# Kernel tuning notes

Hardware: AMD Instinct MI355X
Metric: run time of the kernel (lower is better)

## Reference

```python
import jax, jax.numpy as jnp
import numpy as np

EPS = 1e-6
POSE_W, DEPTH_W, POINTS_W, NORMAL_W = 1.0, 1.0, 1.0, 0.1
DEPTH_MIN = 1e-6


def mat_to_quat(M):
    # pytorch3d-style robust rotation-matrix -> quaternion (w,x,y,z)
    m00, m01, m02 = M[..., 0, 0], M[..., 0, 1], M[..., 0, 2]
    m10, m11, m12 = M[..., 1, 0], M[..., 1, 1], M[..., 1, 2]
    m20, m21, m22 = M[..., 2, 0], M[..., 2, 1], M[..., 2, 2]
    q_abs = jnp.sqrt(jnp.maximum(jnp.stack([
        1.0 + m00 + m11 + m22,
        1.0 + m00 - m11 - m22,
        1.0 - m00 + m11 - m22,
        1.0 - m00 - m11 + m22], axis=-1), 0.0))
    cand = jnp.stack([
        jnp.stack([q_abs[..., 0] ** 2, m21 - m12, m02 - m20, m10 - m01], -1),
        jnp.stack([m21 - m12, q_abs[..., 1] ** 2, m10 + m01, m02 + m20], -1),
        jnp.stack([m02 - m20, m10 + m01, q_abs[..., 2] ** 2, m12 + m21], -1),
        jnp.stack([m10 - m01, m20 + m02, m21 + m12, q_abs[..., 3] ** 2], -1),
    ], axis=-2)  # [...,4,4]
    cand = cand / (2.0 * jnp.maximum(q_abs[..., None], 0.1))
    best = jnp.argmax(q_abs, axis=-1)
    quat = jnp.take_along_axis(cand, best[..., None, None], axis=-2)[..., 0, :]
    return jnp.where(quat[..., 0:1] < 0, -quat, quat)


def pose_encoding(extri, intr, H, W):
    # extri [B,S,3,4] -> [B,S,9] = absT(3) + quat(4) + fov_h,fov_w
    T = extri[..., :3, 3]
    quat = mat_to_quat(extri[..., :3, :3])
    fov_h = 2.0 * jnp.arctan((H / 2.0) / intr[..., 1, 1])
    fov_w = 2.0 * jnp.arctan((W / 2.0) / intr[..., 0, 0])
    return jnp.concatenate([T, quat, fov_h[..., None], fov_w[..., None]], axis=-1)


def align_depth_scale(dp, dg, vm):
    # batched masked-median scale; dp detached by caller. Returns (aligned_gt, scales[B,S])
    B, S, H, W = dg.shape
    dpf, dgf = dp.reshape(B, S, H * W), dg.reshape(B, S, H * W)
    m = vm.reshape(B, S, H * W)
    m2 = m & jnp.isfinite(dpf) & (dpf > EPS)
    ratio = dpf / jnp.maximum(dgf, EPS)
    fm = m2 & jnp.isfinite(ratio)
    msum = m2.sum(-1)
    fcnt = fm.sum(-1)
    r = jnp.sort(jnp.where(fm, ratio, jnp.inf), axis=-1)
    idx = jnp.maximum((fcnt - 1) // 2, 0)  # torch lower median
    med = jnp.take_along_axis(r, idx[..., None], axis=-1)[..., 0]
    scale = jnp.clip(med, 1e-3, 1e3)
    scale = jnp.where((msum < 16) | (fcnt == 0), jnp.ones_like(scale), scale)
    return dg * scale[..., None, None], scale


def _cam_grid(depth, intr):
    B, S, H, W = depth.shape
    ys, xs = jnp.meshgrid(jnp.arange(H, dtype=depth.dtype),
                          jnp.arange(W, dtype=depth.dtype), indexing='ij')
    fx = intr[..., 0, 0][..., None, None]
    fy = intr[..., 1, 1][..., None, None]
    cx = intr[..., 0, 2][..., None, None]
    cy = intr[..., 1, 2][..., None, None]
    x = (xs - cx) / jnp.maximum(fx, EPS) * depth
    y = (ys - cy) / jnp.maximum(fy, EPS) * depth
    return jnp.stack([x, y, depth], axis=-1)  # [B,S,H,W,3]


def depth_to_normals(depth, intr):
    pts = _cam_grid(depth, intr)
    fx_diff = pts[..., 1:-1, 2:, :] - pts[..., 1:-1, :-2, :]
    fy_diff = pts[..., 2:, 1:-1, :] - pts[..., :-2, 1:-1, :]
    core = jnp.cross(fy_diff, fx_diff)
    core = core / jnp.maximum(jnp.linalg.norm(core, axis=-1, keepdims=True), EPS)
    return jnp.zeros_like(pts).at[..., 1:-1, 1:-1, :].set(core)


def depth_to_world_points(depth, intr, pose):
    cam_pts = _cam_grid(depth, intr)
    rot = pose[..., :3, :3]
    trans = pose[..., :3, 3]
    return jnp.einsum('bsij,bshwj->bshwi', rot, cam_pts) + trans[..., None, None, :]


def masked_l1(pred, target, mask):
    mask = mask.astype(pred.dtype)
    return ((pred - target) * mask).__abs__().sum() / jnp.maximum(mask.sum(), 1.0)


def masked_cosine_loss(pred, target, mask):
    pred = pred / jnp.maximum(jnp.linalg.norm(pred, axis=-1, keepdims=True), EPS)
    target = target / jnp.maximum(jnp.linalg.norm(target, axis=-1, keepdims=True), EPS)
    cos = jnp.clip((pred * target).sum(-1), -1.0, 1.0)
    m = mask.astype(cos.dtype)
    return ((1.0 - cos) * m).sum() / jnp.maximum(m.sum(), 1.0)


def smooth_l1(pred, target):
    d = jnp.abs(pred - target)
    return jnp.mean(jnp.where(d < 1.0, 0.5 * d * d, d - 0.5))


def supervised_loss(depth_pred, points_pred, pose_pred, depth_gt, intrinsics,
                    pose_matrix_gt, valid_mask):
    B, S, H, W = depth_gt.shape
    vm = valid_mask & jnp.isfinite(depth_gt) & (depth_gt > DEPTH_MIN)
    depth_gt_aligned, scales = align_depth_scale(
        jax.lax.stop_gradient(depth_pred), depth_gt, vm)
    points_gt = depth_to_world_points(depth_gt_aligned, intrinsics, pose_matrix_gt)
    points_mask = jnp.broadcast_to(vm[..., None], points_gt.shape)
    # normal mask: zero-out 1-pixel border
    border = jnp.zeros((H, W), dtype=bool).at[1:-1, 1:-1].set(True)
    normal_mask = vm & border
    pred_normals = depth_to_normals(depth_pred, intrinsics)
    gt_normals = depth_to_normals(depth_gt, intrinsics)
    normal_loss = masked_cosine_loss(pred_normals, gt_normals, normal_mask)
    pose_gt = pose_encoding(pose_matrix_gt[..., :3, :], intrinsics, H, W)
    pose_gt = pose_gt.at[..., :3].multiply(scales[..., None])
    depth_loss = masked_l1(depth_pred, depth_gt_aligned, vm)
    points_loss = masked_l1(points_pred, points_gt, points_mask)
    pose_loss = smooth_l1(pose_pred, pose_gt)
    return (POSE_W * pose_loss + DEPTH_W * depth_loss
            + POINTS_W * points_loss + NORMAL_W * normal_loss)


def setup_inputs() -> dict:
    key = jax.random.key(0)
    ks = jax.random.split(key, 7)
    B, S, H, W = 4, 8, 384, 512
    depth_gt = jax.random.uniform(ks[0], (B, S, H, W), minval=0.5, maxval=10.0)
    depth_pred = depth_gt * jax.random.uniform(ks[1], (B, S, H, W), minval=0.8, maxval=1.2)
    points_pred = jax.random.normal(ks[2], (B, S, H, W, 3))
    pose_pred = 0.1 * jax.random.normal(ks[3], (B, S, 9))
    intr = jnp.broadcast_to(jnp.array([[500.0, 0.0, W / 2.0],
                                       [0.0, 500.0, H / 2.0],
                                       [0.0, 0.0, 1.0]], jnp.float32), (B, S, 3, 3))
    q, _ = jnp.linalg.qr(jax.random.normal(ks[4], (B, S, 3, 3)))
    R = q * jnp.sign(jnp.linalg.det(q))[..., None, None]  # det=+1
    t = jax.random.normal(ks[5], (B, S, 3))
    top = jnp.concatenate([R, t[..., None]], axis=-1)
    bottom = jnp.broadcast_to(jnp.array([0.0, 0.0, 0.0, 1.0], jnp.float32), (B, S, 1, 4))
    pose_matrix_gt = jnp.concatenate([top, bottom], axis=-2)
    valid_mask = jax.random.uniform(ks[6], (B, S, H, W)) > 0.05
    return {"depth_pred": depth_pred, "points_pred": points_pred,
            "pose_pred": pose_pred, "depth_gt": depth_gt,
            "intrinsics": intr, "pose_matrix_gt": pose_matrix_gt,
            "valid_mask": valid_mask}


def reference(depth_pred, points_pred, pose_pred, depth_gt, intrinsics,
              pose_matrix_gt, valid_mask):
    return supervised_loss(depth_pred, points_pred, pose_pred, depth_gt,
                           intrinsics, pose_matrix_gt, valid_mask)
```

## Files before the change

### kernel.cpp

```cpp
#include <hip/hip_runtime.h>
#include <stdint.h>

#define H_ 384
#define W_ 512
#define HW_ (H_ * W_)
#define NIMG 32
#define EPSF 1e-6f
#define HBLK 16
#define HTHR 512
#define PXB (HW_ / HBLK)
#define CITER (PXB / (HTHR * 4))
#define MBLK 96
#define NPARTS (MBLK * NIMG)
#define SENT 0xFFFFFFFFu

#define OFF_MSUM   0
#define OFF_FCNT   32
#define OFF_KREM1  64
#define OFF_PREF1  96
#define OFF_POSE   128
#define OFF_PMF    160
#define OFF_PNC    1184
#define OFF_PART   2208
#define OFF_PHA    11424
#define OFF_PHB    (OFF_PHA + NIMG*HBLK*2048)

__device__ __forceinline__ bool finitef(float x) {
    return ((__float_as_uint(x) >> 23) & 0xFFu) != 0xFFu;
}

__global__ __launch_bounds__(HTHR) void hist0_k(
    const float* __restrict__ dp, const float* __restrict__ dg,
    const uint8_t* __restrict__ vmask, uint32_t* __restrict__ ws)
{
    __shared__ uint32_t lh[2048];
    __shared__ int sm[8], sf[8];
    const int img = blockIdx.y, blk = blockIdx.x, t = threadIdx.x;
    for (int b = t; b < 2048; b += HTHR) lh[b] = 0;
    __syncthreads();

    const size_t base = (size_t)img * HW_;
    const float* dpi = dp + base;
    const float* dgi = dg + base;
    const uint8_t* mi = vmask + base;

    int m2c = 0, fmc = 0;

    for (int c = 0; c < CITER; ++c) {
        const int pix = blk * PXB + c * (HTHR * 4) + t * 4;
        const float4 v_dp = *reinterpret_cast<const float4*>(dpi + pix);
        const float4 v_dg = *reinterpret_cast<const float4*>(dgi + pix);
        const uchar4 v_m  = *reinterpret_cast<const uchar4*>(mi + pix);
        const float dpa[4] = {v_dp.x, v_dp.y, v_dp.z, v_dp.w};
        const float dga[4] = {v_dg.x, v_dg.y, v_dg.z, v_dg.w};
        const uint8_t ma[4] = {v_m.x, v_m.y, v_m.z, v_m.w};
        int bins[4]; bool fms[4];
#pragma unroll
        for (int e = 0; e < 4; ++e) {
            const float dgv = dga[e], dpv = dpa[e];
            const bool vm = ma[e] && finitef(dgv) && (dgv > 1e-6f);
            const bool m2 = vm && finitef(dpv) && (dpv > EPSF);
            const float ratio = dpv / fmaxf(dgv, EPSF);
            const bool fm = m2 && finitef(ratio);
            m2c += (int)m2; fmc += (int)fm;
            const uint32_t key = fm ? __float_as_uint(ratio) : SENT;
            bins[e] = (int)(key >> 21);
            fms[e] = fm;
        }

#pragma unroll
        for (int e = 0; e < 4; ++e) {
            const bool fm = fms[e];
            const int bin = bins[e];
            unsigned long long todo = __ballot(fm);
            while (todo) {
                const int lead = (int)__ffsll(todo) - 1;
                const int lbin = __shfl(bin, lead);
                const unsigned long long same = __ballot(fm && (bin == lbin));
                if ((t & 63) == lead)
                    atomicAdd(&lh[lbin], (uint32_t)__popcll(same));
                todo &= ~same;
            }
        }
    }

    for (int o = 32; o > 0; o >>= 1) { m2c += __shfl_down(m2c, o); fmc += __shfl_down(fmc, o); }
    if ((t & 63) == 0) { sm[t >> 6] = m2c; sf[t >> 6] = fmc; }
    __syncthreads();
    if (t == 0) {
        int M = 0, F = 0;
        for (int w = 0; w < 8; ++w) { M += sm[w]; F += sf[w]; }
        int* pmf = (int*)(ws + OFF_PMF) + (img * HBLK + blk) * 2;
        pmf[0] = M; pmf[1] = F;
    }

    uint32_t* phb = ws + OFF_PHA + (size_t)(img * HBLK + blk) * 2048;
    for (int b = t; b < 2048; b += HTHR) phb[b] = lh[b];
}

__global__ __launch_bounds__(HTHR) void histp1_k(
    const float* __restrict__ dp, const float* __restrict__ dg,
    const uint8_t* __restrict__ vmask, const float* __restrict__ intr,
    uint32_t* __restrict__ ws)
{
    __shared__ uint32_t lh[256];
    __shared__ uint32_t wsum[8];
    __shared__ int s_bin, s_krem, s_msum, s_fcnt;
    __shared__ float sI[4];
    __shared__ float sns[8]; __shared__ int snc[8];
    const int img = blockIdx.y, blk = blockIdx.x, t = threadIdx.x;

    const uint32_t* pin = ws + OFF_PHA + (size_t)img * HBLK * 2048;
    uint32_t local[4];
#pragma unroll
    for (int c = 0; c < 4; ++c) local[c] = 0;
    for (int b = 0; b < HBLK; ++b) {
        const uint32_t* row = pin + b * 2048 + t * 4;
#pragma unroll
        for (int c = 0; c < 4; ++c) local[c] += row[c];
    }
    const uint32_t cs = local[0] + local[1] + local[2] + local[3];

    uint32_t v = cs;
#pragma unroll
    for (int o = 1; o < 64; o <<= 1) {
        const uint32_t u = __shfl_up(v, o);
        if ((t & 63) >= o) v += u;
    }
    if ((t & 63) == 63) wsum[t >> 6] = v;
    if (t == 0) {
        s_bin = 0; s_krem = 0;
        const int* pmf = (const int*)(ws + OFF_PMF) + img * HBLK * 2;
        int M = 0, F = 0;
        for (int b = 0; b < HBLK; ++b) { M += pmf[2 * b]; F += pmf[2 * b + 1]; }
        s_msum = M; s_fcnt = F;
        sI[0] = 1.0f / fmaxf(intr[img * 9 + 0], EPSF);
        sI[1] = 1.0f / fmaxf(intr[img * 9 + 4], EPSF);
        sI[2] = intr[img * 9 + 2];
        sI[3] = intr[img * 9 + 5];
    }
    __syncthreads();
    uint32_t woff = 0;
    for (int w = 0; w < (t >> 6); ++w) woff += wsum[w];
    const uint32_t incl = woff + v;
    const uint32_t excl = incl - cs;

    const uint32_t k = (uint32_t)max((s_fcnt - 1) / 2, 0);
    if (k >= excl && k < incl) {
        uint32_t cum = excl;
#pragma unroll
        for (int c = 0; c < 4; ++c) {
            if (cum + local[c] > k) { s_bin = t * 4 + c; s_krem = (int)(k - cum); break; }
            cum += local[c];
        }
    }
    __syncthreads();
    if (t == 0 && blk == 0) {
        ((int*)(ws + OFF_MSUM))[img] = s_msum;
        ((int*)(ws + OFF_FCNT))[img] = s_fcnt;
        (ws + OFF_PREF1)[img] = (uint32_t)s_bin << 21;
        ((int*)(ws + OFF_KREM1))[img] = s_krem;
    }
    const uint32_t pm = (uint32_t)s_bin;
    const float inv_fx = sI[0], inv_fy = sI[1], cx = sI[2], cy = sI[3];

    if (t < 256) lh[t] = 0;
    __syncthreads();

    const size_t base = (size_t)img * HW_;
    const float* dpi = dp + base;
    const float* dgi = dg + base;
    float nsum = 0.0f; int ncc = 0;

    for (int c = 0; c < CITER; ++c) {
        const int pix = blk * PXB + c * (HTHR * 4) + t * 4;
        const int i = pix >> 9;
        const int j0 = pix & 511;
        const float4 v_dp = *reinterpret_cast<const float4*>(dpi + pix);
        const float4 v_dg = *reinterpret_cast<const float4*>(dgi + pix);
        const uchar4 v_m  = *reinterpret_cast<const uchar4*>(vmask + base + pix);

        const int im = (i > 0) ? i - 1 : 0;
        const int ip = (i < H_ - 1) ? i + 1 : i;
        const int jme = (j0 > 0) ? j0 - 1 : 0;
        const int jpe = (j0 + 4 < W_) ? j0 + 4 : W_ - 1;
        const float4 dpU = *reinterpret_cast<const float4*>(dpi + im * W_ + j0);
        const float4 dpD = *reinterpret_cast<const float4*>(dpi + ip * W_ + j0);
        const float4 dgU = *reinterpret_cast<const float4*>(dgi + im * W_ + j0);
        const float4 dgD = *reinterpret_cast<const float4*>(dgi + ip * W_ + j0);
        const float dpLe = dpi[i * W_ + jme], dpRe = dpi[i * W_ + jpe];
        const float dgLe = dgi[i * W_ + jme], dgRe = dgi[i * W_ + jpe];

        const float dpa[4] = {v_dp.x, v_dp.y, v_dp.z, v_dp.w};
        const float dga[4] = {v_dg.x, v_dg.y, v_dg.z, v_dg.w};
        const float dpUa[4] = {dpU.x, dpU.y, dpU.z, dpU.w};
        const float dpDa[4] = {dpD.x, dpD.y, dpD.z, dpD.w};
        const float dgUa[4] = {dgU.x, dgU.y, dgU.z, dgU.w};
        const float dgDa[4] = {dgD.x, dgD.y, dgD.z, dgD.w};
        const uint8_t ma[4] = {v_m.x, v_m.y, v_m.z, v_m.w};

        const float ay = ((float)i - cy) * inv_fy;
        const bool row_int = (i >= 1) && (i <= H_ - 2);

#pragma unroll
        for (int e = 0; e < 4; ++e) {
            const int j = j0 + e;
            const float dgv = dga[e], dpv = dpa[e];
            const bool vm = ma[e] && finitef(dgv) && (dgv > 1e-6f);
            const bool m2 = vm && finitef(dpv) && (dpv > EPSF);
            const float ratio = dpv / fmaxf(dgv, EPSF);
            const bool fm = m2 && finitef(ratio);
            const uint32_t key = fm ? __float_as_uint(ratio) : SENT;
            if ((key >> 21) == pm)
                atomicAdd(&lh[(key >> 13) & 255u], 1u);

            const bool nm = vm && row_int && (j >= 1) && (j <= W_ - 2);
            const float pdL = (e == 0) ? dpLe : dpa[e - 1];
            const float pdR = (e == 3) ? dpRe : dpa[e + 1];
            const float gdL = (e == 0) ? dgLe : dga[e - 1];
            const float gdR = (e == 3) ? dgRe : dga[e + 1];
            const float pdU = dpUa[e], pdD = dpDa[e];
            const float gdU = dgUa[e], gdD = dgDa[e];
            const float ax = ((float)j - cx) * inv_fx;

            const float dRLp = pdR - pdL, dDUp = pdD - pdU;
            const float Ap = inv_fy * (pdD + pdU);
            const float Bp = inv_fx * (pdR + pdL);
            const float cpx = dRLp * Ap;
            const float cpy = dDUp * Bp;
            const float cpz = -(Ap * Bp + ax * cpx + ay * cpy);
            const float dRLg = gdR - gdL, dDUg = gdD - gdU;
            const float Ag = inv_fy * (gdD + gdU);
            const float Bg = inv_fx * (gdR + gdL);
            const float cgx = dRLg * Ag;
            const float cgy = dDUg * Bg;
            const float cgz = -(Ag * Bg + ax * cgx + ay * cgy);

            const float np2 = cpx * cpx + cpy * cpy + cpz * cpz;
            const float ng2 = cgx * cgx + cgy * cgy + cgz * cgz;
            const float dpg = cpx * cgx + cpy * cgy + cpz * cgz;
            const float den = fmaxf(np2, 1e-12f) * fmaxf(ng2, 1e-12f);
            float cosv = dpg * __builtin_amdgcn_rsqf(den);
            cosv = fminf(fmaxf(cosv, -1.0f), 1.0f);
            nsum += nm ? (1.0f - cosv) : 0.0f;
            ncc  += nm ? 1 : 0;
        }
    }
    __syncthreads();

    uint32_t* pout = ws + OFF_PHB + (size_t)(img * HBLK + blk) * 256;
    if (t < 256) pout[t] = lh[t];

    for (int o = 32; o > 0; o >>= 1) { nsum += __shfl_down(nsum, o); ncc += __shfl_down(ncc, o); }
    if ((t & 63) == 0) { sns[t >> 6] = nsum; snc[t >> 6] = ncc; }
    __syncthreads();
    if (t == 0) {
        float NS = 0.0f; int NC = 0;
        for (int w = 0; w < 8; ++w) { NS += sns[w]; NC += snc[w]; }
        float* pnc = (float*)(ws + OFF_PNC) + (img * HBLK + blk) * 2;
        pnc[0] = NS; pnc[1] = (float)NC;
    }
}

__global__ __launch_bounds__(256) void main_loss(
    const float* __restrict__ dp, const float* __restrict__ dg,
    const uint8_t* __restrict__ vmask, const float* __restrict__ pts_pred,
    const float* __restrict__ intr, const float* __restrict__ posegt,
    const float* __restrict__ posepred, uint32_t* __restrict__ ws)
{
    const int img = blockIdx.y;
    const int t = threadIdx.x;

    const size_t base = (size_t)img * HW_;
    const int pix0 = (blockIdx.x * 256 + t) * 8;
    const int i = pix0 >> 9;
    const int j0 = pix0 & 511;
    const float4 dpC0 = *reinterpret_cast<const float4*>(dp + base + pix0);
    const float4 dpC1 = *reinterpret_cast<const float4*>(dp + base + pix0 + 4);
    const float4 dgC0 = *reinterpret_cast<const float4*>(dg + base + pix0);
    const float4 dgC1 = *reinterpret_cast<const float4*>(dg + base + pix0 + 4);
    const uchar4 m0 = *reinterpret_cast<const uchar4*>(vmask + base + pix0);
    const uchar4 m1 = *reinterpret_cast<const uchar4*>(vmask + base + pix0 + 4);
    const float4 pp0 = *reinterpret_cast<const float4*>(pts_pred + (base + pix0) * 3);
    const float4 pp1 = *reinterpret_cast<const float4*>(pts_pred + (base + pix0) * 3 + 4);
    const float4 pp2 = *reinterpret_cast<const float4*>(pts_pred + (base + pix0) * 3 + 8);
    const float4 pp3 = *reinterpret_cast<const float4*>(pts_pred + (base + pix0) * 3 + 12);
    const float4 pp4 = *reinterpret_cast<const float4*>(pts_pred + (base + pix0) * 3 + 16);
    const float4 pp5 = *reinterpret_cast<const float4*>(pts_pred + (base + pix0) * 3 + 20);

    __shared__ uint32_t wsum[4];
    __shared__ int s_bin;
    __shared__ float sP[17];
    {
        const uint32_t* ph = ws + OFF_PHB + (size_t)img * HBLK * 256;
        uint32_t cs = 0;
        for (int b = 0; b < HBLK; ++b) cs += ph[b * 256 + t];
        uint32_t v = cs;
#pragma unroll
        for (int o = 1; o < 64; o <<= 1) {
            const uint32_t u = __shfl_up(v, o);
            if ((t & 63) >= o) v += u;
        }
        if ((t & 63) == 63) wsum[t >> 6] = v;
        if (t == 0) s_bin = 0;
        __syncthreads();
        uint32_t woff = 0;
        for (int w = 0; w < (t >> 6); ++w) woff += wsum[w];
        const uint32_t incl = woff + v;
        const uint32_t excl = incl - cs;
        const uint32_t k = (uint32_t)((const int*)(ws + OFF_KREM1))[img];
        if (k >= excl && k < incl) s_bin = t;
        __syncthreads();
    }
    if (t == 0) {
        const uint32_t med_u = (ws + OFF_PREF1)[img] | ((uint32_t)s_bin << 13) | 4096u;
        float sc_ = fminf(fmaxf(__uint_as_float(med_u), 0.001f), 1000.0f);
        const int fcnt = ((const int*)(ws + OFF_FCNT))[img];
        const int msum = ((const int*)(ws + OFF_MSUM))[img];
        if (msum < 16 || fcnt == 0) sc_ = 1.0f;

        const float* p = posegt + img * 16;
        sP[0] = p[0]; sP[1] = p[1]; sP[2] = p[2];  sP[9]  = p[3];
        sP[3] = p[4]; sP[4] = p[5]; sP[5] = p[6];  sP[10] = p[7];
        sP[6] = p[8]; sP[7] = p[9]; sP[8] = p[10]; sP[11] = p[11];
        sP[12] = intr[img * 9 + 0]; sP[13] = intr[img * 9 + 4];
        sP[14] = intr[img * 9 + 2]; sP[15] = intr[img * 9 + 5];
        sP[16] = sc_;

        if (blockIdx.x == 0) {
            const float m00 = p[0], m01 = p[1], m02 = p[2], tx = p[3];
            const float m10 = p[4], m11 = p[5], m12 = p[6], ty = p[7];
            const float m20 = p[8], m21 = p[9], m22 = p[10], tz = p[11];
            float qa[4];
            qa[0] = sqrtf(fmaxf(1.0f + m00 + m11 + m22, 0.0f));
            qa[1] = sqrtf(fmaxf(1.0f + m00 - m11 - m22, 0.0f));
            qa[2] = sqrtf(fmaxf(1.0f - m00 + m11 - m22, 0.0f));
            qa[3] = sqrtf(fmaxf(1.0f - m00 - m11 + m22, 0.0f));
            int best = 0; float bv = qa[0];
            for (int i2 = 1; i2 < 4; ++i2) if (qa[i2] > bv) { bv = qa[i2]; best = i2; }
            float c0, c1, c2, c3;
            if (best == 0)      { c0 = qa[0]*qa[0]; c1 = m21 - m12;   c2 = m02 - m20;   c3 = m10 - m01; }
            else if (best == 1) { c0 = m21 - m12;   c1 = qa[1]*qa[1]; c2 = m10 + m01;   c3 = m02 + m20; }
            else if (best == 2) { c0 = m02 - m20;   c1 = m10 + m01;   c2 = qa[2]*qa[2]; c3 = m12 + m21; }
            else                { c0 = m10 - m01;   c1 = m20 + m02;   c2 = m21 + m12;   c3 = qa[3]*qa[3]; }
            const float denom = 2.0f * fmaxf(qa[best], 0.1f);
            float q0 = c0 / denom, q1 = c1 / denom, q2 = c2 / denom, q3 = c3 / denom;
            if (q0 < 0.0f) { q0 = -q0; q1 = -q1; q2 = -q2; q3 = -q3; }
            const float fovh = 2.0f * atanf((H_ * 0.5f) / sP[13]);
            const float fovw = 2.0f * atanf((W_ * 0.5f) / sP[12]);
            const float pg[9] = {tx * sc_, ty * sc_, tz * sc_, q0, q1, q2, q3, fovh, fovw};
            const float* ppred = posepred + img * 9;
            float s = 0.0f;
            for (int i2 = 0; i2 < 9; ++i2) {
                const float d = fabsf(ppred[i2] - pg[i2]);
                s += (d < 1.0f) ? 0.5f * d * d : d - 0.5f;
            }
            ((float*)(ws + OFF_POSE))[img] = s;
        }
    }
    __syncthreads();
    const float R00 = sP[0], R01 = sP[1], R02 = sP[2];
    const float R10 = sP[3], R11 = sP[4], R12 = sP[5];
    const float R20 = sP[6], R21 = sP[7], R22 = sP[8];
    const float T0 = sP[9], T1 = sP[10], T2 = sP[11];
    const float inv_fx = 1.0f / fmaxf(sP[12], EPSF);
    const float inv_fy = 1.0f / fmaxf(sP[13], EPSF);
    const float cx = sP[14], cy = sP[15];
    const float sc = sP[16];

    const float ppv[24] = {pp0.x, pp0.y, pp0.z, pp0.w, pp1.x, pp1.y, pp1.z, pp1.w,
                           pp2.x, pp2.y, pp2.z, pp2.w, pp3.x, pp3.y, pp3.z, pp3.w,
                           pp4.x, pp4.y, pp4.z, pp4.w, pp5.x, pp5.y, pp5.z, pp5.w};
    const float dpa[8] = {dpC0.x, dpC0.y, dpC0.z, dpC0.w, dpC1.x, dpC1.y, dpC1.z, dpC1.w};
    const float dga[8] = {dgC0.x, dgC0.y, dgC0.z, dgC0.w, dgC1.x, dgC1.y, dgC1.z, dgC1.w};
    const uint8_t ma[8] = {m0.x, m0.y, m0.z, m0.w, m1.x, m1.y, m1.z, m1.w};

    const float ay = ((float)i - cy) * inv_fy;

    float dsum = 0.0f, psum = 0.0f, vcnt = 0.0f;
#pragma unroll
    for (int e = 0; e < 8; ++e) {
        const int j = j0 + e;
        const float dgv = dga[e], dpv = dpa[e];
        const bool vm = ma[e] && finitef(dgv) && (dgv > 1e-6f);
        vcnt += vm ? 1.0f : 0.0f;
        const float dal = dgv * sc;
        dsum += vm ? fabsf(dpv - dal) : 0.0f;
        const float ax = ((float)j - cx) * inv_fx;
        const float cxx = ax * dal, cyy = ay * dal;
        const float wx = R00 * cxx + R01 * cyy + R02 * dal + T0;
        const float wy = R10 * cxx + R11 * cyy + R12 * dal + T1;
        const float wz = R20 * cxx + R21 * cyy + R22 * dal + T2;
        const float pl = fabsf(ppv[3 * e] - wx) + fabsf(ppv[3 * e + 1] - wy)
                       + fabsf(ppv[3 * e + 2] - wz);
        psum += vm ? pl : 0.0f;
    }

    float vals[3] = {vcnt, dsum, psum};
    __shared__ float red[4][3];
    const int wave = t >> 6, lane = t & 63;
#pragma unroll
    for (int q = 0; q < 3; ++q) {
        float v = vals[q];
        for (int o = 32; o > 0; o >>= 1) v += __shfl_down(v, o);
        if (lane == 0) red[wave][q] = v;
    }
    __syncthreads();
    if (t == 0) {
        const int slot = blockIdx.y * gridDim.x + blockIdx.x;
        float* part = (float*)(ws + OFF_PART) + slot * 3;
#pragma unroll
        for (int q = 0; q < 3; ++q)
            part[q] = red[0][q] + red[1][q] + red[2][q] + red[3][q];
    }
}

__global__ __launch_bounds__(256) void finalize_k(const uint32_t* __restrict__ ws,
                                                  float* __restrict__ out)
{
    const float* part = (const float*)(ws + OFF_PART);
    const int t = threadIdx.x;
    double s0 = 0, s1 = 0, s2 = 0, sn = 0, sc2 = 0;
    for (int slot = t; slot < NPARTS; slot += 256) {
        s0 += (double)part[slot * 3 + 0];
        s1 += (double)part[slot * 3 + 1];
        s2 += (double)part[slot * 3 + 2];
    }
    const float* pnc = (const float*)(ws + OFF_PNC);
    for (int slot = t; slot < NIMG * HBLK; slot += 256) {
        sn  += (double)pnc[slot * 2 + 0];
        sc2 += (double)pnc[slot * 2 + 1];
    }
    __shared__ double red[4][5];
    const int wave = t >> 6, lane = t & 63;
    double dv[5] = {s0, s1, s2, sn, sc2};
#pragma unroll
    for (int q = 0; q < 5; ++q) {
        double v = dv[q];
        for (int o = 32; o > 0; o >>= 1) v += __shfl_down(v, o);
        if (lane == 0) red[wave][q] = v;
    }
    __syncthreads();
    if (t == 0) {
        double tot[5];
#pragma unroll
        for (int q = 0; q < 5; ++q)
            tot[q] = red[0][q] + red[1][q] + red[2][q] + red[3][q];
        const float* pose = (const float*)(ws + OFF_POSE);
        double ps = 0.0;
        for (int i2 = 0; i2 < NIMG; ++i2) ps += (double)pose[i2];
        const double vmc = tot[0];
        const double depth_loss  = tot[1] / fmax(vmc, 1.0);
        const double points_loss = tot[2] / fmax(3.0 * vmc, 1.0);
        const double normal_loss = tot[3] / fmax(tot[4], 1.0);
        const double pose_loss   = ps / 288.0;
        out[0] = (float)(pose_loss + depth_loss + points_loss + 0.1 * normal_loss);
    }
}

extern "C" void kernel_launch(void* const* d_in, const int* in_sizes, int n_in,
                              void* d_out, int out_size, void* d_ws, size_t ws_size,
                              hipStream_t stream)
{
    const float*   dp       = (const float*)d_in[0];
    const float*   pts_pred = (const float*)d_in[1];
    const float*   posepred = (const float*)d_in[2];
    const float*   dg       = (const float*)d_in[3];
    const float*   intr     = (const float*)d_in[4];
    const float*   posegt   = (const float*)d_in[5];
    const uint8_t* vmask    = (const uint8_t*)d_in[6];
    float* out = (float*)d_out;
    uint32_t* ws = (uint32_t*)d_ws;

    const dim3 hgrid(HBLK, NIMG);
    hist0_k<<<hgrid, HTHR, 0, stream>>>(dp, dg, vmask, ws);
    histp1_k<<<hgrid, HTHR, 0, stream>>>(dp, dg, vmask, intr, ws);
    main_loss<<<dim3(MBLK, NIMG), 256, 0, stream>>>(dp, dg, vmask, pts_pred, intr, posegt,
                                                     posepred, ws);
    finalize_k<<<1, 256, 0, stream>>>(ws, out);
}
```

Measured before the change: 72.92 us.

## Move normal loss to first pass and hoist median selection into dedicated kernel

Moves the normal-consistency computation from the second histogram pass into the first, and widens the second-level histogram from 256 to 2048 bins. A new per-image kernel now does the median bin selection, scale and pose loss once, instead of every main_loss block redoing the 256-bin scan. This lightens main_loss and histp1 but adds a kernel launch and larger histogram writes and reads.

```diff
diff --git a/kernel.cpp b/kernel.cpp
--- a/kernel.cpp
+++ b/kernel.cpp
@@ -18,11 +18,12 @@
 #define OFF_FCNT   32
 #define OFF_KREM1  64
 #define OFF_PREF1  96
-#define OFF_POSE   128
-#define OFF_PMF    160
-#define OFF_PNC    1184
-#define OFF_PART   2208
-#define OFF_PHA    11424
+#define OFF_SCALE  128
+#define OFF_POSE   160
+#define OFF_PMF    192
+#define OFF_PNC    1216
+#define OFF_PART   2240
+#define OFF_PHA    11456
 #define OFF_PHB    (OFF_PHA + NIMG*HBLK*2048)
 
 __device__ __forceinline__ bool finitef(float x) {
@@ -31,32 +32,67 @@
 
 __global__ __launch_bounds__(HTHR) void hist0_k(
     const float* __restrict__ dp, const float* __restrict__ dg,
-    const uint8_t* __restrict__ vmask, uint32_t* __restrict__ ws)
+    const uint8_t* __restrict__ vmask, const float* __restrict__ intr,
+    uint32_t* __restrict__ ws)
 {
     __shared__ uint32_t lh[2048];
-    __shared__ int sm[8], sf[8];
+    __shared__ int sm[8], sf[8], snc[8];
+    __shared__ float sns[8];
+    __shared__ float sI[4];
     const int img = blockIdx.y, blk = blockIdx.x, t = threadIdx.x;
     for (int b = t; b < 2048; b += HTHR) lh[b] = 0;
-    __syncthreads();
+    if (t == 0) {
+        sI[0] = 1.0f / fmaxf(intr[img * 9 + 0], EPSF);
+        sI[1] = 1.0f / fmaxf(intr[img * 9 + 4], EPSF);
+        sI[2] = intr[img * 9 + 2];
+        sI[3] = intr[img * 9 + 5];
+    }
+    __syncthreads();
+    const float inv_fx = sI[0], inv_fy = sI[1], cx = sI[2], cy = sI[3];
 
     const size_t base = (size_t)img * HW_;
     const float* dpi = dp + base;
     const float* dgi = dg + base;
     const uint8_t* mi = vmask + base;
 
-    int m2c = 0, fmc = 0;
+    int m2c = 0, fmc = 0, ncc = 0;
+    float nsum = 0.0f;
 
     for (int c = 0; c < CITER; ++c) {
         const int pix = blk * PXB + c * (HTHR * 4) + t * 4;
+        const int i = pix >> 9;
+        const int j0 = pix & 511;
+
         const float4 v_dp = *reinterpret_cast<const float4*>(dpi + pix);
         const float4 v_dg = *reinterpret_cast<const float4*>(dgi + pix);
         const uchar4 v_m  = *reinterpret_cast<const uchar4*>(mi + pix);
+
+        const int im = (i > 0) ? i - 1 : 0;
+        const int ip = (i < H_ - 1) ? i + 1 : i;
+        const int jme = (j0 > 0) ? j0 - 1 : 0;
+        const int jpe = (j0 + 4 < W_) ? j0 + 4 : W_ - 1;
+        const float4 dpU = *reinterpret_cast<const float4*>(dpi + im * W_ + j0);
+        const float4 dpD = *reinterpret_cast<const float4*>(dpi + ip * W_ + j0);
+        const float4 dgU = *reinterpret_cast<const float4*>(dgi + im * W_ + j0);
+        const float4 dgD = *reinterpret_cast<const float4*>(dgi + ip * W_ + j0);
+        const float dpLe = dpi[i * W_ + jme], dpRe = dpi[i * W_ + jpe];
+        const float dgLe = dgi[i * W_ + jme], dgRe = dgi[i * W_ + jpe];
+
         const float dpa[4] = {v_dp.x, v_dp.y, v_dp.z, v_dp.w};
         const float dga[4] = {v_dg.x, v_dg.y, v_dg.z, v_dg.w};
+        const float dpUa[4] = {dpU.x, dpU.y, dpU.z, dpU.w};
+        const float dpDa[4] = {dpD.x, dpD.y, dpD.z, dpD.w};
+        const float dgUa[4] = {dgU.x, dgU.y, dgU.z, dgU.w};
+        const float dgDa[4] = {dgD.x, dgD.y, dgD.z, dgD.w};
         const uint8_t ma[4] = {v_m.x, v_m.y, v_m.z, v_m.w};
+
+        const float ay = ((float)i - cy) * inv_fy;
+        const bool row_int = (i >= 1) && (i <= H_ - 2);
+
         int bins[4]; bool fms[4];
 #pragma unroll
         for (int e = 0; e < 4; ++e) {
+            const int j = j0 + e;
             const float dgv = dga[e], dpv = dpa[e];
             const bool vm = ma[e] && finitef(dgv) && (dgv > 1e-6f);
             const bool m2 = vm && finitef(dpv) && (dpv > EPSF);
@@ -66,6 +102,37 @@
             const uint32_t key = fm ? __float_as_uint(ratio) : SENT;
             bins[e] = (int)(key >> 21);
             fms[e] = fm;
+
+            const bool nm = vm && row_int && (j >= 1) && (j <= W_ - 2);
+            const float pdL = (e == 0) ? dpLe : dpa[e - 1];
+            const float pdR = (e == 3) ? dpRe : dpa[e + 1];
+            const float gdL = (e == 0) ? dgLe : dga[e - 1];
+            const float gdR = (e == 3) ? dgRe : dga[e + 1];
+            const float pdU = dpUa[e], pdD = dpDa[e];
+            const float gdU = dgUa[e], gdD = dgDa[e];
+            const float ax = ((float)j - cx) * inv_fx;
+
+            const float dRLp = pdR - pdL, dDUp = pdD - pdU;
+            const float Ap = inv_fy * (pdD + pdU);
+            const float Bp = inv_fx * (pdR + pdL);
+            const float cpx = dRLp * Ap;
+            const float cpy = dDUp * Bp;
+            const float cpz = -(Ap * Bp + ax * cpx + ay * cpy);
+            const float dRLg = gdR - gdL, dDUg = gdD - gdU;
+            const float Ag = inv_fy * (gdD + gdU);
+            const float Bg = inv_fx * (gdR + gdL);
+            const float cgx = dRLg * Ag;
+            const float cgy = dDUg * Bg;
+            const float cgz = -(Ag * Bg + ax * cgx + ay * cgy);
+
+            const float np2 = cpx * cpx + cpy * cpy + cpz * cpz;
+            const float ng2 = cgx * cgx + cgy * cgy + cgz * cgz;
+            const float dpg = cpx * cgx + cpy * cgy + cpz * cgz;
+            const float den = fmaxf(np2, 1e-12f) * fmaxf(ng2, 1e-12f);
+            float cosv = dpg * __builtin_amdgcn_rsqf(den);
+            cosv = fminf(fmaxf(cosv, -1.0f), 1.0f);
+            nsum += nm ? (1.0f - cosv) : 0.0f;
+            ncc  += nm ? 1 : 0;
         }
 
 #pragma unroll
@@ -84,14 +151,19 @@
         }
     }
 
-    for (int o = 32; o > 0; o >>= 1) { m2c += __shfl_down(m2c, o); fmc += __shfl_down(fmc, o); }
-    if ((t & 63) == 0) { sm[t >> 6] = m2c; sf[t >> 6] = fmc; }
-    __syncthreads();
-    if (t == 0) {
-        int M = 0, F = 0;
-        for (int w = 0; w < 8; ++w) { M += sm[w]; F += sf[w]; }
+    for (int o = 32; o > 0; o >>= 1) {
+        m2c += __shfl_down(m2c, o); fmc += __shfl_down(fmc, o);
+        nsum += __shfl_down(nsum, o); ncc += __shfl_down(ncc, o);
+    }
+    if ((t & 63) == 0) { sm[t >> 6] = m2c; sf[t >> 6] = fmc; sns[t >> 6] = nsum; snc[t >> 6] = ncc; }
+    __syncthreads();
+    if (t == 0) {
+        int M = 0, F = 0, NC = 0; float NS = 0.0f;
+        for (int w = 0; w < 8; ++w) { M += sm[w]; F += sf[w]; NS += sns[w]; NC += snc[w]; }
         int* pmf = (int*)(ws + OFF_PMF) + (img * HBLK + blk) * 2;
         pmf[0] = M; pmf[1] = F;
+        float* pnc = (float*)(ws + OFF_PNC) + (img * HBLK + blk) * 2;
+        pnc[0] = NS; pnc[1] = (float)NC;
     }
 
     uint32_t* phb = ws + OFF_PHA + (size_t)(img * HBLK + blk) * 2048;
@@ -100,14 +172,11 @@
 
 __global__ __launch_bounds__(HTHR) void histp1_k(
     const float* __restrict__ dp, const float* __restrict__ dg,
-    const uint8_t* __restrict__ vmask, const float* __restrict__ intr,
-    uint32_t* __restrict__ ws)
+    const uint8_t* __restrict__ vmask, uint32_t* __restrict__ ws)
 {
-    __shared__ uint32_t lh[256];
+    __shared__ uint32_t lh[2048];
     __shared__ uint32_t wsum[8];
     __shared__ int s_bin, s_krem, s_msum, s_fcnt;
-    __shared__ float sI[4];
-    __shared__ float sns[8]; __shared__ int snc[8];
     const int img = blockIdx.y, blk = blockIdx.x, t = threadIdx.x;
 
     const uint32_t* pin = ws + OFF_PHA + (size_t)img * HBLK * 2048;
@@ -134,10 +203,6 @@
         int M = 0, F = 0;
         for (int b = 0; b < HBLK; ++b) { M += pmf[2 * b]; F += pmf[2 * b + 1]; }
         s_msum = M; s_fcnt = F;
-        sI[0] = 1.0f / fmaxf(intr[img * 9 + 0], EPSF);
-        sI[1] = 1.0f / fmaxf(intr[img * 9 + 4], EPSF);
-        sI[2] = intr[img * 9 + 2];
-        sI[3] = intr[img * 9 + 5];
     }
     __syncthreads();
     uint32_t woff = 0;
@@ -162,49 +227,21 @@
         ((int*)(ws + OFF_KREM1))[img] = s_krem;
     }
     const uint32_t pm = (uint32_t)s_bin;
-    const float inv_fx = sI[0], inv_fy = sI[1], cx = sI[2], cy = sI[3];
-
-    if (t < 256) lh[t] = 0;
+
+    for (int b = t; b < 2048; b += HTHR) lh[b] = 0;
     __syncthreads();
 
     const size_t base = (size_t)img * HW_;
-    const float* dpi = dp + base;
-    const float* dgi = dg + base;
-    float nsum = 0.0f; int ncc = 0;
-
     for (int c = 0; c < CITER; ++c) {
         const int pix = blk * PXB + c * (HTHR * 4) + t * 4;
-        const int i = pix >> 9;
-        const int j0 = pix & 511;
-        const float4 v_dp = *reinterpret_cast<const float4*>(dpi + pix);
-        const float4 v_dg = *reinterpret_cast<const float4*>(dgi + pix);
+        const float4 v_dp = *reinterpret_cast<const float4*>(dp + base + pix);
+        const float4 v_dg = *reinterpret_cast<const float4*>(dg + base + pix);
         const uchar4 v_m  = *reinterpret_cast<const uchar4*>(vmask + base + pix);
-
-        const int im = (i > 0) ? i - 1 : 0;
-        const int ip = (i < H_ - 1) ? i + 1 : i;
-        const int jme = (j0 > 0) ? j0 - 1 : 0;
-        const int jpe = (j0 + 4 < W_) ? j0 + 4 : W_ - 1;
-        const float4 dpU = *reinterpret_cast<const float4*>(dpi + im * W_ + j0);
-        const float4 dpD = *reinterpret_cast<const float4*>(dpi + ip * W_ + j0);
-        const float4 dgU = *reinterpret_cast<const float4*>(dgi + im * W_ + j0);
-        const float4 dgD = *reinterpret_cast<const float4*>(dgi + ip * W_ + j0);
-        const float dpLe = dpi[i * W_ + jme], dpRe = dpi[i * W_ + jpe];
-        const float dgLe = dgi[i * W_ + jme], dgRe = dgi[i * W_ + jpe];
-
         const float dpa[4] = {v_dp.x, v_dp.y, v_dp.z, v_dp.w};
         const float dga[4] = {v_dg.x, v_dg.y, v_dg.z, v_dg.w};
-        const float dpUa[4] = {dpU.x, dpU.y, dpU.z, dpU.w};
-        const float dpDa[4] = {dpD.x, dpD.y, dpD.z, dpD.w};
-        const float dgUa[4] = {dgU.x, dgU.y, dgU.z, dgU.w};
-        const float dgDa[4] = {dgD.x, dgD.y, dgD.z, dgD.w};
         const uint8_t ma[4] = {v_m.x, v_m.y, v_m.z, v_m.w};
-
-        const float ay = ((float)i - cy) * inv_fy;
-        const bool row_int = (i >= 1) && (i <= H_ - 2);
-
 #pragma unroll
         for (int e = 0; e < 4; ++e) {
-            const int j = j0 + e;
             const float dgv = dga[e], dpv = dpa[e];
             const bool vm = ma[e] && finitef(dgv) && (dgv > 1e-6f);
             const bool m2 = vm && finitef(dpv) && (dpv > EPSF);
@@ -212,53 +249,101 @@
             const bool fm = m2 && finitef(ratio);
             const uint32_t key = fm ? __float_as_uint(ratio) : SENT;
             if ((key >> 21) == pm)
-                atomicAdd(&lh[(key >> 13) & 255u], 1u);
-
-            const bool nm = vm && row_int && (j >= 1) && (j <= W_ - 2);
-            const float pdL = (e == 0) ? dpLe : dpa[e - 1];
-            const float pdR = (e == 3) ? dpRe : dpa[e + 1];
-            const float gdL = (e == 0) ? dgLe : dga[e - 1];
-            const float gdR = (e == 3) ? dgRe : dga[e + 1];
-            const float pdU = dpUa[e], pdD = dpDa[e];
-            const float gdU = dgUa[e], gdD = dgDa[e];
-            const float ax = ((float)j - cx) * inv_fx;
-
-            const float dRLp = pdR - pdL, dDUp = pdD - pdU;
-            const float Ap = inv_fy * (pdD + pdU);
-            const float Bp = inv_fx * (pdR + pdL);
-            const float cpx = dRLp * Ap;
-            const float cpy = dDUp * Bp;
-            const float cpz = -(Ap * Bp + ax * cpx + ay * cpy);
-            const float dRLg = gdR - gdL, dDUg = gdD - gdU;
-            const float Ag = inv_fy * (gdD + gdU);
-            const float Bg = inv_fx * (gdR + gdL);
-            const float cgx = dRLg * Ag;
-            const float cgy = dDUg * Bg;
-            const float cgz = -(Ag * Bg + ax * cgx + ay * cgy);
-
-            const float np2 = cpx * cpx + cpy * cpy + cpz * cpz;
-            const float ng2 = cgx * cgx + cgy * cgy + cgz * cgz;
-            const float dpg = cpx * cgx + cpy * cgy + cpz * cgz;
-            const float den = fmaxf(np2, 1e-12f) * fmaxf(ng2, 1e-12f);
-            float cosv = dpg * __builtin_amdgcn_rsqf(den);
-            cosv = fminf(fmaxf(cosv, -1.0f), 1.0f);
-            nsum += nm ? (1.0f - cosv) : 0.0f;
-            ncc  += nm ? 1 : 0;
+                atomicAdd(&lh[(key >> 10) & 2047u], 1u);
         }
     }
     __syncthreads();
 
-    uint32_t* pout = ws + OFF_PHB + (size_t)(img * HBLK + blk) * 256;
-    if (t < 256) pout[t] = lh[t];
-
-    for (int o = 32; o > 0; o >>= 1) { nsum += __shfl_down(nsum, o); ncc += __shfl_down(ncc, o); }
-    if ((t & 63) == 0) { sns[t >> 6] = nsum; snc[t >> 6] = ncc; }
-    __syncthreads();
-    if (t == 0) {
-        float NS = 0.0f; int NC = 0;
-        for (int w = 0; w < 8; ++w) { NS += sns[w]; NC += snc[w]; }
-        float* pnc = (float*)(ws + OFF_PNC) + (img * HBLK + blk) * 2;
-        pnc[0] = NS; pnc[1] = (float)NC;
+    uint32_t* pout = ws + OFF_PHB + (size_t)(img * HBLK + blk) * 2048;
+    for (int b = t; b < 2048; b += HTHR) pout[b] = lh[b];
+}
+
+__global__ __launch_bounds__(256) void sel_mid_k(
+    uint32_t* __restrict__ ws,
+    const float* __restrict__ intr, const float* __restrict__ posegt,
+    const float* __restrict__ posepred)
+{
+    const int img = blockIdx.x;
+    const int t = threadIdx.x;
+    const uint32_t* ph = ws + OFF_PHB + (size_t)img * HBLK * 2048;
+    uint32_t local[8];
+#pragma unroll
+    for (int c = 0; c < 8; ++c) local[c] = 0;
+    for (int b = 0; b < HBLK; ++b) {
+        const uint32_t* row = ph + b * 2048 + t * 8;
+#pragma unroll
+        for (int c = 0; c < 8; ++c) local[c] += row[c];
+    }
+    uint32_t cs = 0;
+#pragma unroll
+    for (int c = 0; c < 8; ++c) cs += local[c];
+
+    __shared__ uint32_t wsum[4];
+    __shared__ int s_bin;
+    uint32_t v = cs;
+#pragma unroll
+    for (int o = 1; o < 64; o <<= 1) {
+        const uint32_t u = __shfl_up(v, o);
+        if ((t & 63) >= o) v += u;
+    }
+    if ((t & 63) == 63) wsum[t >> 6] = v;
+    if (t == 0) s_bin = 0;
+    __syncthreads();
+    uint32_t woff = 0;
+    for (int w = 0; w < (t >> 6); ++w) woff += wsum[w];
+    const uint32_t incl = woff + v;
+    const uint32_t excl = incl - cs;
+
+    const uint32_t k = (uint32_t)((const int*)(ws + OFF_KREM1))[img];
+    if (k >= excl && k < incl) {
+        uint32_t cum = excl;
+#pragma unroll
+        for (int c = 0; c < 8; ++c) {
+            if (cum + local[c] > k) { s_bin = t * 8 + c; break; }
+            cum += local[c];
+        }
+    }
+    __syncthreads();
+
+    if (t == 0) {
+        const uint32_t med_u = (ws + OFF_PREF1)[img] | ((uint32_t)s_bin << 10) | 512u;
+        const float med = __uint_as_float(med_u);
+        float sc_ = fminf(fmaxf(med, 0.001f), 1000.0f);
+        const int fcnt = ((const int*)(ws + OFF_FCNT))[img];
+        const int msum = ((const int*)(ws + OFF_MSUM))[img];
+        if (msum < 16 || fcnt == 0) sc_ = 1.0f;
+        ((float*)(ws + OFF_SCALE))[img] = sc_;
+
+        const float* p = posegt + img * 16;
+        const float m00 = p[0], m01 = p[1], m02 = p[2], tx = p[3];
+        const float m10 = p[4], m11 = p[5], m12 = p[6], ty = p[7];
+        const float m20 = p[8], m21 = p[9], m22 = p[10], tz = p[11];
+        float qa[4];
+        qa[0] = sqrtf(fmaxf(1.0f + m00 + m11 + m22, 0.0f));
+        qa[1] = sqrtf(fmaxf(1.0f + m00 - m11 - m22, 0.0f));
+        qa[2] = sqrtf(fmaxf(1.0f - m00 + m11 - m22, 0.0f));
+        qa[3] = sqrtf(fmaxf(1.0f - m00 - m11 + m22, 0.0f));
+        int best = 0; float bv = qa[0];
+        for (int i2 = 1; i2 < 4; ++i2) if (qa[i2] > bv) { bv = qa[i2]; best = i2; }
+        float c0, c1, c2, c3;
+        if (best == 0)      { c0 = qa[0]*qa[0]; c1 = m21 - m12;   c2 = m02 - m20;   c3 = m10 - m01; }
+        else if (best == 1) { c0 = m21 - m12;   c1 = qa[1]*qa[1]; c2 = m10 + m01;   c3 = m02 + m20; }
+        else if (best == 2) { c0 = m02 - m20;   c1 = m10 + m01;   c2 = qa[2]*qa[2]; c3 = m12 + m21; }
+        else                { c0 = m10 - m01;   c1 = m20 + m02;   c2 = m21 + m12;   c3 = qa[3]*qa[3]; }
+        const float denom = 2.0f * fmaxf(qa[best], 0.1f);
+        float q0 = c0 / denom, q1 = c1 / denom, q2 = c2 / denom, q3 = c3 / denom;
+        if (q0 < 0.0f) { q0 = -q0; q1 = -q1; q2 = -q2; q3 = -q3; }
+        const float fx = intr[img * 9 + 0], fy = intr[img * 9 + 4];
+        const float fovh = 2.0f * atanf((H_ * 0.5f) / fy);
+        const float fovw = 2.0f * atanf((W_ * 0.5f) / fx);
+        const float pg[9] = {tx * sc_, ty * sc_, tz * sc_, q0, q1, q2, q3, fovh, fovw};
+        const float* ppred = posepred + img * 9;
+        float s = 0.0f;
+        for (int i2 = 0; i2 < 9; ++i2) {
+            const float d = fabsf(ppred[i2] - pg[i2]);
+            s += (d < 1.0f) ? 0.5f * d * d : d - 0.5f;
+        }
+        ((float*)(ws + OFF_POSE))[img] = s;
     }
 }
 
@@ -266,7 +351,7 @@
     const float* __restrict__ dp, const float* __restrict__ dg,
     const uint8_t* __restrict__ vmask, const float* __restrict__ pts_pred,
     const float* __restrict__ intr, const float* __restrict__ posegt,
-    const float* __restrict__ posepred, uint32_t* __restrict__ ws)
+    uint32_t* __restrict__ ws)
 {
     const int img = blockIdx.y;
     const int t = threadIdx.x;
@@ -288,75 +373,15 @@
     const float4 pp4 = *reinterpret_cast<const float4*>(pts_pred + (base + pix0) * 3 + 16);
     const float4 pp5 = *reinterpret_cast<const float4*>(pts_pred + (base + pix0) * 3 + 20);
 
-    __shared__ uint32_t wsum[4];
-    __shared__ int s_bin;
     __shared__ float sP[17];
-    {
-        const uint32_t* ph = ws + OFF_PHB + (size_t)img * HBLK * 256;
-        uint32_t cs = 0;
-        for (int b = 0; b < HBLK; ++b) cs += ph[b * 256 + t];
-        uint32_t v = cs;
-#pragma unroll
-        for (int o = 1; o < 64; o <<= 1) {
-            const uint32_t u = __shfl_up(v, o);
-            if ((t & 63) >= o) v += u;
-        }
-        if ((t & 63) == 63) wsum[t >> 6] = v;
-        if (t == 0) s_bin = 0;
-        __syncthreads();
-        uint32_t woff = 0;
-        for (int w = 0; w < (t >> 6); ++w) woff += wsum[w];
-        const uint32_t incl = woff + v;
-        const uint32_t excl = incl - cs;
-        const uint32_t k = (uint32_t)((const int*)(ws + OFF_KREM1))[img];
-        if (k >= excl && k < incl) s_bin = t;
-        __syncthreads();
-    }
-    if (t == 0) {
-        const uint32_t med_u = (ws + OFF_PREF1)[img] | ((uint32_t)s_bin << 13) | 4096u;
-        float sc_ = fminf(fmaxf(__uint_as_float(med_u), 0.001f), 1000.0f);
-        const int fcnt = ((const int*)(ws + OFF_FCNT))[img];
-        const int msum = ((const int*)(ws + OFF_MSUM))[img];
-        if (msum < 16 || fcnt == 0) sc_ = 1.0f;
-
+    if (t == 0) {
         const float* p = posegt + img * 16;
         sP[0] = p[0]; sP[1] = p[1]; sP[2] = p[2];  sP[9]  = p[3];
         sP[3] = p[4]; sP[4] = p[5]; sP[5] = p[6];  sP[10] = p[7];
         sP[6] = p[8]; sP[7] = p[9]; sP[8] = p[10]; sP[11] = p[11];
         sP[12] = intr[img * 9 + 0]; sP[13] = intr[img * 9 + 4];
         sP[14] = intr[img * 9 + 2]; sP[15] = intr[img * 9 + 5];
-        sP[16] = sc_;
-
-        if (blockIdx.x == 0) {
-            const float m00 = p[0], m01 = p[1], m02 = p[2], tx = p[3];
-            const float m10 = p[4], m11 = p[5], m12 = p[6], ty = p[7];
-            const float m20 = p[8], m21 = p[9], m22 = p[10], tz = p[11];
-            float qa[4];
-            qa[0] = sqrtf(fmaxf(1.0f + m00 + m11 + m22, 0.0f));
-            qa[1] = sqrtf(fmaxf(1.0f + m00 - m11 - m22, 0.0f));
-            qa[2] = sqrtf(fmaxf(1.0f - m00 + m11 - m22, 0.0f));
-            qa[3] = sqrtf(fmaxf(1.0f - m00 - m11 + m22, 0.0f));
-            int best = 0; float bv = qa[0];
-            for (int i2 = 1; i2 < 4; ++i2) if (qa[i2] > bv) { bv = qa[i2]; best = i2; }
-            float c0, c1, c2, c3;
-            if (best == 0)      { c0 = qa[0]*qa[0]; c1 = m21 - m12;   c2 = m02 - m20;   c3 = m10 - m01; }
-            else if (best == 1) { c0 = m21 - m12;   c1 = qa[1]*qa[1]; c2 = m10 + m01;   c3 = m02 + m20; }
-            else if (best == 2) { c0 = m02 - m20;   c1 = m10 + m01;   c2 = qa[2]*qa[2]; c3 = m12 + m21; }
-            else                { c0 = m10 - m01;   c1 = m20 + m02;   c2 = m21 + m12;   c3 = qa[3]*qa[3]; }
-            const float denom = 2.0f * fmaxf(qa[best], 0.1f);
-            float q0 = c0 / denom, q1 = c1 / denom, q2 = c2 / denom, q3 = c3 / denom;
-            if (q0 < 0.0f) { q0 = -q0; q1 = -q1; q2 = -q2; q3 = -q3; }
-            const float fovh = 2.0f * atanf((H_ * 0.5f) / sP[13]);
-            const float fovw = 2.0f * atanf((W_ * 0.5f) / sP[12]);
-            const float pg[9] = {tx * sc_, ty * sc_, tz * sc_, q0, q1, q2, q3, fovh, fovw};
-            const float* ppred = posepred + img * 9;
-            float s = 0.0f;
-            for (int i2 = 0; i2 < 9; ++i2) {
-                const float d = fabsf(ppred[i2] - pg[i2]);
-                s += (d < 1.0f) ? 0.5f * d * d : d - 0.5f;
-            }
-            ((float*)(ws + OFF_POSE))[img] = s;
-        }
+        sP[16] = ((const float*)(ws + OFF_SCALE))[img];
     }
     __syncthreads();
     const float R00 = sP[0], R01 = sP[1], R02 = sP[2];
@@ -473,9 +498,9 @@
     uint32_t* ws = (uint32_t*)d_ws;
 
     const dim3 hgrid(HBLK, NIMG);
-    hist0_k<<<hgrid, HTHR, 0, stream>>>(dp, dg, vmask, ws);
-    histp1_k<<<hgrid, HTHR, 0, stream>>>(dp, dg, vmask, intr, ws);
-    main_loss<<<dim3(MBLK, NIMG), 256, 0, stream>>>(dp, dg, vmask, pts_pred, intr, posegt,
-                                                     posepred, ws);
+    hist0_k<<<hgrid, HTHR, 0, stream>>>(dp, dg, vmask, intr, ws);
+    histp1_k<<<hgrid, HTHR, 0, stream>>>(dp, dg, vmask, ws);
+    sel_mid_k<<<NIMG, 256, 0, stream>>>(ws, intr, posegt, posepred);
+    main_loss<<<dim3(MBLK, NIMG), 256, 0, stream>>>(dp, dg, vmask, pts_pred, intr, posegt, ws);
     finalize_k<<<1, 256, 0, stream>>>(ws, out);
 }
```

New measurement: 72.07 us. Within noise of the previous version (-1.2%).
